# Kernel optimization log

Hardware: AMD Instinct MI355X
Metric: run time of the kernel (lower is better)

## Reference

```python
import jax, jax.numpy as jnp
import numpy as np

N = 50000          # total nodes
B = 10             # graphs in batch
NPG = N // B       # nodes per graph (equal-sized graphs)
E = 800000         # edges
IN_DIM = 128
HID = 128
NHEAD = 4
DHEAD = HID // NHEAD
T = 1000
SLOPE = 0.2        # leaky_relu negative slope
ALPHA_L = 2.0


def _ln(x, g=None, b=None, eps=1e-5):
    mu = jnp.mean(x, axis=-1, keepdims=True)
    var = jnp.var(x, axis=-1, keepdims=True)
    y = (x - mu) * jax.lax.rsqrt(var + eps)
    if g is not None:
        y = y * g + b
    return y


def _gatv2(h, src, dst, Ws, Wd, a, b):
    # DGL GATv2Conv, share_weights=False, residual=False, bias=True, activation=gelu
    fs = (h @ Ws).reshape(N, NHEAD, DHEAD)
    fd = (h @ Wd).reshape(N, NHEAD, DHEAD)
    # per-edge attention logits [E, NHEAD]
    e = jnp.sum(jax.nn.leaky_relu(fs[src] + fd[dst], SLOPE) * a, axis=-1)
    # edge softmax grouped by destination node
    m = jax.ops.segment_max(e, dst, num_segments=N)
    ee = jnp.exp(e - m[dst])
    den = jax.ops.segment_sum(ee, dst, num_segments=N)
    alpha = ee / den[dst]                                  # [E, NHEAD]
    rst = jax.ops.segment_sum(alpha[..., None] * fs[src], dst, num_segments=N)
    rst = jax.nn.gelu(rst + b.reshape(1, NHEAD, DHEAD), approximate=False)
    return rst.reshape(N, HID)


def _forward(x, noise, sab, somab, time_emb,
             Ws0, Wd0, a0, b0, g0, be0,
             Ws1, Wd1, a1, b1, g1, be1,
             Wo1, bo1, Wo2, bo2, src, dst, t):
    # sample_q: statistics-matched signed noise
    miu = jnp.mean(x, axis=0)
    std = jnp.std(x, axis=0, ddof=1)          # torch.std is unbiased
    nz = _ln(noise) * std + miu
    nz = jnp.sign(x) * jnp.abs(nz)
    s1 = jnp.repeat(sab[t], NPG)[:, None]
    s2 = jnp.repeat(somab[t], NPG)[:, None]
    x_t = s1 * x + s2 * nz
    temb = jnp.repeat(time_emb[t], NPG, axis=0)
    # Denoising_Unet
    h = jnp.concatenate([x_t, temb], axis=1)   # [N, IN_DIM+HID]
    h = _ln(_gatv2(h, src, dst, Ws0, Wd0, a0, b0), g0, be0)
    h_in = h
    h = _gatv2(h, src, dst, Ws1, Wd1, a1, b1)
    h = _ln(h + h_in, g1, be1)                 # residual (shapes match)
    out = jax.nn.relu(h @ Wo1 + bo1) @ Wo2 + bo2
    # loss_fn
    mse = jnp.mean((out - x) ** 2)
    on = out / jnp.maximum(jnp.linalg.norm(out, axis=-1, keepdims=True), 1e-12)
    xn = x / jnp.maximum(jnp.linalg.norm(x, axis=-1, keepdims=True), 1e-12)
    cos = jnp.mean((1.0 - jnp.sum(on * xn, axis=-1)) ** ALPHA_L)
    return mse + 0.1 * cos


def setup_inputs() -> dict:
    key = jax.random.key(0)
    ks = jax.random.split(key, 26)
    betas = np.linspace(1e-4, 0.02, T, dtype=np.float64)
    ab = np.cumprod(1.0 - betas)
    s = 0.02
    in0 = IN_DIM + HID
    inp = {}
    inp['x'] = jax.random.normal(ks[0], (N, IN_DIM), jnp.float32)
    inp['noise'] = jax.random.normal(ks[1], (N, IN_DIM), jnp.float32)
    inp['src'] = jax.random.randint(ks[2], (E,), 0, N, dtype=jnp.int32)
    inp['dst'] = jax.random.randint(ks[3], (E,), 0, N, dtype=jnp.int32)
    inp['t'] = jax.random.randint(ks[4], (B,), 0, T, dtype=jnp.int32)
    inp['sab'] = jnp.asarray(np.sqrt(ab), jnp.float32)
    inp['somab'] = jnp.asarray(np.sqrt(1.0 - ab), jnp.float32)
    inp['time_emb'] = jax.random.normal(ks[5], (T, HID), jnp.float32) * s
    inp['Ws0'] = jax.random.normal(ks[6], (in0, HID), jnp.float32) * s
    inp['Wd0'] = jax.random.normal(ks[7], (in0, HID), jnp.float32) * s
    inp['a0'] = jax.random.normal(ks[8], (NHEAD, DHEAD), jnp.float32) * s
    inp['b0'] = jnp.zeros((HID,), jnp.float32)
    inp['g0'] = jnp.ones((HID,), jnp.float32)
    inp['be0'] = jnp.zeros((HID,), jnp.float32)
    inp['Ws1'] = jax.random.normal(ks[9], (HID, HID), jnp.float32) * s
    inp['Wd1'] = jax.random.normal(ks[10], (HID, HID), jnp.float32) * s
    inp['a1'] = jax.random.normal(ks[11], (NHEAD, DHEAD), jnp.float32) * s
    inp['b1'] = jnp.zeros((HID,), jnp.float32)
    inp['g1'] = jnp.ones((HID,), jnp.float32)
    inp['be1'] = jnp.zeros((HID,), jnp.float32)
    inp['Wo1'] = jax.random.normal(ks[12], (HID, HID), jnp.float32) * s
    inp['bo1'] = jnp.zeros((HID,), jnp.float32)
    inp['Wo2'] = jax.random.normal(ks[13], (HID, IN_DIM), jnp.float32) * s
    inp['bo2'] = jnp.zeros((IN_DIM,), jnp.float32)
    return inp


def reference(x, noise, src, dst, t, sab, somab, time_emb,
              Ws0, Wd0, a0, b0, g0, be0,
              Ws1, Wd1, a1, b1, g1, be1,
              Wo1, bo1, Wo2, bo2):
    return _forward(x, noise, sab, somab, time_emb,
                    Ws0, Wd0, a0, b0, g0, be0,
                    Ws1, Wd1, a1, b1, g1, be1,
                    Wo1, bo1, Wo2, bo2, src, dst, t)
```

## Files before the change

kernel.cpp:

```cpp
#include <hip/hip_runtime.h>
#include <hip/hip_bf16.h>
#include <math.h>

#define NN 50000
#define EE 800000
#define NPG 5000

typedef short bf16x8 __attribute__((ext_vector_type(8)));
typedef float f32x4 __attribute__((ext_vector_type(4)));

__device__ __forceinline__ float gelu_exact(float v) {
    return 0.5f * v * (1.0f + erff(v * 0.70710678118654752440f));
}

__device__ __forceinline__ ushort f2b(float f) {
    union { float f; uint u; } v; v.f = f;
    uint r = (v.u + 0x7fffu + ((v.u >> 16) & 1)) >> 16;
    return (ushort)r;
}
__device__ __forceinline__ uint pack2(float a, float b) {
    return (uint)f2b(a) | ((uint)f2b(b) << 16);
}
__device__ __forceinline__ float blo(uint u) {
    union { uint u; float f; } v; v.u = u << 16; return v.f;
}
__device__ __forceinline__ float bhi(uint u) {
    union { uint u; float f; } v; v.u = u & 0xffff0000u; return v.f;
}
__device__ __forceinline__ void unpack8(uint4 u, float* f) {
    f[0] = blo(u.x); f[1] = bhi(u.x); f[2] = blo(u.y); f[3] = bhi(u.y);
    f[4] = blo(u.z); f[5] = bhi(u.z); f[6] = blo(u.w); f[7] = bhi(u.w);
}

__global__ __launch_bounds__(256) void head1_kernel(const float* __restrict__ x,
        float* __restrict__ sums, const int* __restrict__ dst, int* __restrict__ counts,
        const float* __restrict__ Ws0, const float* __restrict__ Wd0,
        const float* __restrict__ Ws1, const float* __restrict__ Wd1,
        const float* __restrict__ Wo1, const float* __restrict__ Wo2,
        ushort* __restrict__ Wt0, ushort* __restrict__ Wt1,
        ushort* __restrict__ Wo1t, ushort* __restrict__ Wo2t) {
    int bid = blockIdx.x;
    int tid = threadIdx.x;
    if (bid < 1024) {
        int col4 = (tid & 31) * 4;
        int rowgrp = tid >> 5;
        float s0 = 0.f, s1 = 0.f, s2 = 0.f, s3 = 0.f;
        float q0 = 0.f, q1 = 0.f, q2 = 0.f, q3 = 0.f;
        for (int r = bid * 8 + rowgrp; r < NN; r += 8192) {
            float4 v = *(const float4*)(x + (size_t)r * 128 + col4);
            s0 += v.x; s1 += v.y; s2 += v.z; s3 += v.w;
            q0 += v.x * v.x; q1 += v.y * v.y; q2 += v.z * v.z; q3 += v.w * v.w;
        }
        s0 += __shfl_xor(s0, 32); s1 += __shfl_xor(s1, 32);
        s2 += __shfl_xor(s2, 32); s3 += __shfl_xor(s3, 32);
        q0 += __shfl_xor(q0, 32); q1 += __shfl_xor(q1, 32);
        q2 += __shfl_xor(q2, 32); q3 += __shfl_xor(q3, 32);
        __shared__ float red[4][32][8];
        int wv = tid >> 6, l = tid & 63;
        if (l < 32) {
            float* p = red[wv][l];
            p[0] = s0; p[1] = s1; p[2] = s2; p[3] = s3;
            p[4] = q0; p[5] = q1; p[6] = q2; p[7] = q3;
        }
        __syncthreads();
        if (tid < 32) {
            float a0 = 0.f, a1 = 0.f, a2 = 0.f, a3 = 0.f;
            float b0 = 0.f, b1 = 0.f, b2 = 0.f, b3 = 0.f;
#pragma unroll
            for (int w = 0; w < 4; ++w) {
                float* p = red[w][tid];
                a0 += p[0]; a1 += p[1]; a2 += p[2]; a3 += p[3];
                b0 += p[4]; b1 += p[5]; b2 += p[6]; b3 += p[7];
            }
            int c = tid * 4;
            atomicAdd(&sums[c], a0); atomicAdd(&sums[c + 1], a1);
            atomicAdd(&sums[c + 2], a2); atomicAdd(&sums[c + 3], a3);
            atomicAdd(&sums[128 + c], b0); atomicAdd(&sums[128 + c + 1], b1);
            atomicAdd(&sums[128 + c + 2], b2); atomicAdd(&sums[128 + c + 3], b3);
        }
    } else if (bid < 4149) {
        int i = (bid - 1024) * 256 + tid;
        if (i < EE) atomicAdd(&counts[dst[i]], 1);
    } else {
        int i = (bid - 4149) * 256 + tid;
        if (i < 65536) {
            int c = i >> 8, k = i & 255;
            const float* W = (c < 128) ? Ws0 : Wd0;
            Wt0[c * 256 + k] = f2b(W[k * 128 + (c & 127)]);
        } else if (i < 98304) {
            int j = i - 65536;
            int c = j >> 7, k = j & 127;
            const float* W = (c < 128) ? Ws1 : Wd1;
            Wt1[c * 128 + k] = f2b(W[k * 128 + (c & 127)]);
        } else if (i < 114688) {
            int j = i - 98304;
            int c = j >> 7, k = j & 127;
            Wo1t[c * 128 + k] = f2b(Wo1[k * 128 + c]);
        } else if (i < 131072) {
            int j = i - 114688;
            int c = j >> 7, k = j & 127;
            Wo2t[c * 128 + k] = f2b(Wo2[k * 128 + c]);
        }
    }
}

__global__ __launch_bounds__(1024) void head2_kernel(const int* __restrict__ counts,
        int* __restrict__ blockSums, float* __restrict__ stats, int n) {
    int bid = blockIdx.x;
    int tid = threadIdx.x;
    if (bid < 49) {
        int i = bid * 1024 + tid;
        int v = (i < n) ? counts[i] : 0;
#pragma unroll
        for (int o = 32; o > 0; o >>= 1) v += __shfl_down(v, o);
        __shared__ int sh[16];
        int lane = tid & 63, wv = tid >> 6;
        if (lane == 0) sh[wv] = v;
        __syncthreads();
        if (tid == 0) {
            int s = 0;
#pragma unroll
            for (int k = 0; k < 16; ++k) s += sh[k];
            blockSums[bid] = s;
        }
    } else {
        if (tid < 128) {
            int c = tid;
            float sum = stats[c], sumsq = stats[128 + c];
            float mu = sum / (float)n;
            float var = (sumsq - sum * sum / (float)n) / (float)(n - 1);
            stats[256 + c] = mu;
            stats[384 + c] = sqrtf(fmaxf(var, 0.f));
        }
    }
}

__global__ __launch_bounds__(1024) void head3_kernel(const float* __restrict__ x,
        const float* __restrict__ noise, const int* __restrict__ t,
        const float* __restrict__ sab, const float* __restrict__ somab,
        const float* __restrict__ temb, const float* __restrict__ stats,
        ushort* __restrict__ h,
        const int* __restrict__ counts, const int* __restrict__ blockSums,
        int* __restrict__ indptr, int* __restrict__ cursor, int n) {
    int bid = blockIdx.x;
    int tid = threadIdx.x;
    if (bid < 3125) {
        int wid = bid * 16 + (tid >> 6);
        int lane = tid & 63;
        int tt = t[wid / NPG];
        float s1 = sab[tt], s2v = somab[tt];
        float2 nz = ((const float2*)noise)[(size_t)wid * 64 + lane];
        float s = nz.x + nz.y;
        float sq = nz.x * nz.x + nz.y * nz.y;
#pragma unroll
        for (int o = 1; o < 64; o <<= 1) { s += __shfl_xor(s, o); sq += __shfl_xor(sq, o); }
        float mu = s * (1.f / 128.f);
        float var = sq * (1.f / 128.f) - mu * mu;
        float r = rsqrtf(var + 1e-5f);
        int f0 = 2 * lane, f1 = f0 + 1;
        float y0 = (nz.x - mu) * r * stats[384 + f0] + stats[256 + f0];
        float y1 = (nz.y - mu) * r * stats[384 + f1] + stats[256 + f1];
        float2 xv = ((const float2*)x)[(size_t)wid * 64 + lane];
        float sg0 = (xv.x > 0.f) ? 1.f : ((xv.x < 0.f) ? -1.f : 0.f);
        float sg1 = (xv.y > 0.f) ? 1.f : ((xv.y < 0.f) ? -1.f : 0.f);
        float n0 = sg0 * fabsf(y0);
        float n1 = sg1 * fabsf(y1);
        float xt0 = s1 * xv.x + s2v * n0;
        float xt1 = s1 * xv.y + s2v * n1;
        uint* row = (uint*)(h + (size_t)wid * 256);
        row[lane] = pack2(xt0, xt1);
        float2 te = ((const float2*)(temb + (size_t)tt * 128))[lane];
        row[64 + lane] = pack2(te.x, te.y);
    } else {
        int b = bid - 3125;
        __shared__ int sOff, sTot;
        if (tid < 64) {
            int v = (tid < 49) ? blockSums[tid] : 0;
            int incl = v;
#pragma unroll
            for (int o = 1; o < 64; o <<= 1) {
                int tv = __shfl_up(incl, o);
                if ((tid & 63) >= o) incl += tv;
            }
            int off = (b == 0) ? 0 : __shfl(incl, b - 1);
            int tot = __shfl(incl, 48);
            if (tid == 0) { sOff = off; sTot = tot; }
        }
        __syncthreads();
        int i = b * 1024 + tid;
        int v = (i < n) ? counts[i] : 0;
        int lane = tid & 63, wv = tid >> 6;
        int incl = v;
#pragma unroll
        for (int o = 1; o < 64; o <<= 1) {
            int tv = __shfl_up(incl, o);
            if (lane >= o) incl += tv;
        }
        __shared__ int wsum[16];
        __shared__ int woff[16];
        if (lane == 63) wsum[wv] = incl;
        __syncthreads();
        if (tid == 0) {
            int s = 0;
#pragma unroll
            for (int k = 0; k < 16; ++k) { woff[k] = s; s += wsum[k]; }
        }
        __syncthreads();
        int ex = incl - v + woff[wv] + sOff;
        if (i < n) { indptr[i] = ex; cursor[i] = ex; }
        if (b == 48 && tid == 0) indptr[n] = sTot;
    }
}

__global__ __launch_bounds__(1024) void scatter_kernel(const int* __restrict__ src,
        const int* __restrict__ dst, int* __restrict__ cursor,
        int* __restrict__ csr_src, int e) {
    int i = blockIdx.x * 1024 + threadIdx.x;
    if (i < e) {
        int p = atomicAdd(&cursor[dst[i]], 1);
        csr_src[p] = src[i];
    }
}

template<int K, int NCOL, int EPI>
__global__ __launch_bounds__(256, 2) void mfma_gemm(const ushort* __restrict__ A,
        const ushort* __restrict__ Wt, const float* __restrict__ bias,
        ushort* __restrict__ C0, ushort* __restrict__ C1,
        const float* __restrict__ X, float* __restrict__ lossAcc, int M) {
    constexpr int NFRAG = NCOL / 16;
    constexpr int KSTEPS = K / 32;
    __shared__ ushort Bs[32 * NCOL];
    int tid = threadIdx.x;
    int wave = tid >> 6, lane = tid & 63;
    int l15 = lane & 15, g = lane >> 4;
    int rowBase = blockIdx.x * 64 + wave * 16;
    int r = rowBase + l15;
    int rc = min(r, M - 1);
    const ushort* Arow = A + (size_t)rc * K + g * 8;

    f32x4 acc[NFRAG] = {};

    for (int ks = 0; ks < KSTEPS; ++ks) {
#pragma unroll
        for (int i = 0; i < NCOL / 64; ++i) {
            int ch = tid + i * 256;
            int c = ch >> 2, q = ch & 3;
            float4 v = *(const float4*)(Wt + (size_t)c * K + ks * 32 + q * 8);
            int off = c * 64 + ((q * 16) ^ ((c & 7) << 4));
            *(float4*)((char*)Bs + off) = v;
        }
        __syncthreads();
        bf16x8 af = *(const bf16x8*)(Arow + ks * 32);
        int roff = l15 * 64 + ((g * 16) ^ ((l15 & 7) << 4));
#pragma unroll
        for (int n = 0; n < NFRAG; ++n) {
            bf16x8 bf = *(const bf16x8*)((const char*)Bs + n * 1024 + roff);
            acc[n] = __builtin_amdgcn_mfma_f32_16x16x32_bf16(af, bf, acc[n], 0, 0, 0);
        }
        __syncthreads();
    }

    if (EPI != 3) {
#pragma unroll
        for (int n = 0; n < NFRAG; ++n) {
            int col = n * 16 + l15;
#pragma unroll
            for (int j = 0; j < 4; ++j) {
                int row = rowBase + g * 4 + j;
                if (row < M) {
                    float v = acc[n][j];
                    if (EPI == 1) v = fmaxf(v + bias[col], 0.f);
                    ushort bv = f2b(v);
                    if (NCOL == 256) {
                        if (n < 8) C0[(size_t)row * 128 + col] = bv;
                        else       C1[(size_t)row * 128 + col - 128] = bv;
                    } else {
                        C0[(size_t)row * 128 + col] = bv;
                    }
                }
            }
        }
    } else {
        float td2 = 0.f, tcl = 0.f;
#pragma unroll
        for (int j = 0; j < 4; ++j) {
            int row = rowBase + g * 4 + j;
            bool rv = row < M;
            float d2 = 0.f, oo = 0.f, xx = 0.f, ox = 0.f;
#pragma unroll
            for (int n = 0; n < NFRAG; ++n) {
                int col = n * 16 + l15;
                float o = rv ? (acc[n][j] + bias[col]) : 0.f;
                float xv = rv ? X[(size_t)row * 128 + col] : 0.f;
                float e = o - xv;
                d2 += e * e; oo += o * o; xx += xv * xv; ox += o * xv;
            }
#pragma unroll
            for (int off = 1; off < 16; off <<= 1) {
                d2 += __shfl_xor(d2, off); oo += __shfl_xor(oo, off);
                xx += __shfl_xor(xx, off); ox += __shfl_xor(ox, off);
            }
            if (rv) {
                float no = fmaxf(sqrtf(oo), 1e-12f);
                float nx = fmaxf(sqrtf(xx), 1e-12f);
                float cs = 1.f - ox / (no * nx);
                td2 += d2; tcl += cs * cs;
            }
        }
        __shared__ float sd2[16], scl[16];
        if (l15 == 0) { sd2[wave * 4 + g] = td2; scl[wave * 4 + g] = tcl; }
        __syncthreads();
        if (tid == 0) {
            float a2 = 0.f, ac = 0.f;
#pragma unroll
            for (int k2 = 0; k2 < 16; ++k2) { a2 += sd2[k2]; ac += scl[k2]; }
            atomicAdd(&lossAcc[0], a2);
            atomicAdd(&lossAcc[1], ac);
        }
    }
}

__global__ __launch_bounds__(256) void gat_ln_kernel(const ushort* __restrict__ fs,
        const ushort* __restrict__ fd, const float* __restrict__ a,
        const float* __restrict__ bias, const int* __restrict__ indptr,
        const int* __restrict__ csr_src, const ushort* __restrict__ residB,
        const float* __restrict__ g, const float* __restrict__ be,
        ushort* __restrict__ outB, int n) {
    int wid = (blockIdx.x * blockDim.x + threadIdx.x) >> 6;
    int lane = threadIdx.x & 63;
    if (wid >= n) return;
    int quad = lane >> 4, s = lane & 15;
    int beg = indptr[wid], cnt = indptr[wid + 1] - beg;
    const int* ip = csr_src + beg;
    const uint4* fs4 = (const uint4*)fs;

    uint4 fdq = ((const uint4*)fd)[(size_t)wid * 16 + s];
    float fdv[8]; unpack8(fdq, fdv);
    float av[8];
    {
        float4 a0 = *(const float4*)(a + 8 * s);
        float4 a1 = *(const float4*)(a + 8 * s + 4);
        av[0] = a0.x; av[1] = a0.y; av[2] = a0.z; av[3] = a0.w;
        av[4] = a1.x; av[5] = a1.y; av[6] = a1.z; av[7] = a1.w;
    }

    int i0 = (quad < cnt) ? ip[quad] : 0;
    int i1 = (4 + quad < cnt) ? ip[4 + quad] : 0;
    uint4 vA = fs4[(size_t)i0 * 16 + s];
    uint4 vB = fs4[(size_t)i1 * 16 + s];
    int p0 = (8  < cnt) ? ip[8]  : 0;
    int p1 = (9  < cnt) ? ip[9]  : 0;
    int p2 = (10 < cnt) ? ip[10] : 0;
    int p3 = (11 < cnt) ? ip[11] : 0;

    float den = 0.f;
    float acc[8] = {};
    for (int j = 0; j < cnt; j += 4) {
        uint4 cur = vA; vA = vB;
        int pe = (quad == 0) ? p0 : (quad == 1) ? p1 : (quad == 2) ? p2 : p3;
        vB = fs4[(size_t)pe * 16 + s];
        p0 = (j + 12 < cnt) ? ip[j + 12] : 0;
        p1 = (j + 13 < cnt) ? ip[j + 13] : 0;
        p2 = (j + 14 < cnt) ? ip[j + 14] : 0;
        p3 = (j + 15 < cnt) ? ip[j + 15] : 0;
        float c[8]; unpack8(cur, c);
        float p = 0.f;
#pragma unroll
        for (int i = 0; i < 8; ++i) {
            float tv = c[i] + fdv[i];
            tv = (tv > 0.f) ? tv : 0.2f * tv;
            p = fmaf(tv, av[i], p);
        }
        p += __shfl_xor(p, 1);
        p += __shfl_xor(p, 2);
        float w = (j + quad < cnt) ? __expf(p) : 0.f;
        den += w;
#pragma unroll
        for (int i = 0; i < 8; ++i) acc[i] = fmaf(w, c[i], acc[i]);
    }
#pragma unroll
    for (int i = 0; i < 8; ++i) {
        acc[i] += __shfl_xor(acc[i], 16);
        acc[i] += __shfl_xor(acc[i], 32);
    }
    den += __shfl_xor(den, 16);
    den += __shfl_xor(den, 32);
    float inv = (cnt > 0) ? 1.f / den : 0.f;

    float bi[8];
    {
        float4 b0v = *(const float4*)(bias + 8 * s);
        float4 b1v = *(const float4*)(bias + 8 * s + 4);
        bi[0] = b0v.x; bi[1] = b0v.y; bi[2] = b0v.z; bi[3] = b0v.w;
        bi[4] = b1v.x; bi[5] = b1v.y; bi[6] = b1v.z; bi[7] = b1v.w;
    }
    float r[8];
#pragma unroll
    for (int i = 0; i < 8; ++i) r[i] = gelu_exact(acc[i] * inv + bi[i]);
    if (residB) {
        uint4 rq = ((const uint4*)residB)[(size_t)wid * 16 + s];
        float rv[8]; unpack8(rq, rv);
#pragma unroll
        for (int i = 0; i < 8; ++i) r[i] += rv[i];
    }
    float ssum = 0.f, ssq = 0.f;
#pragma unroll
    for (int i = 0; i < 8; ++i) { ssum += r[i]; ssq += r[i] * r[i]; }
#pragma unroll
    for (int o = 1; o < 16; o <<= 1) { ssum += __shfl_xor(ssum, o); ssq += __shfl_xor(ssq, o); }
    float mu = ssum * (1.f / 128.f);
    float var = ssq * (1.f / 128.f) - mu * mu;
    float rstd = rsqrtf(var + 1e-5f);
    float gv[8], bv[8];
    {
        float4 g0v = *(const float4*)(g + 8 * s);
        float4 g1v = *(const float4*)(g + 8 * s + 4);
        gv[0] = g0v.x; gv[1] = g0v.y; gv[2] = g0v.z; gv[3] = g0v.w;
        gv[4] = g1v.x; gv[5] = g1v.y; gv[6] = g1v.z; gv[7] = g1v.w;
        float4 e0v = *(const float4*)(be + 8 * s);
        float4 e1v = *(const float4*)(be + 8 * s + 4);
        bv[0] = e0v.x; bv[1] = e0v.y; bv[2] = e0v.z; bv[3] = e0v.w;
        bv[4] = e1v.x; bv[5] = e1v.y; bv[6] = e1v.z; bv[7] = e1v.w;
    }
    float o_[8];
#pragma unroll
    for (int i = 0; i < 8; ++i) o_[i] = (r[i] - mu) * rstd * gv[i] + bv[i];
    if (quad == 0) {
        uint4 w4;
        w4.x = pack2(o_[0], o_[1]); w4.y = pack2(o_[2], o_[3]);
        w4.z = pack2(o_[4], o_[5]); w4.w = pack2(o_[6], o_[7]);
        ((uint4*)outB)[(size_t)wid * 16 + s] = w4;
    }
}

__global__ void loss_final2(const float* __restrict__ lossAcc, float* __restrict__ outp, int n) {
    outp[0] = lossAcc[0] / ((float)n * 128.f) + 0.1f * (lossAcc[1] / (float)n);
}

extern "C" void kernel_launch(void* const* d_in, const int* in_sizes, int n_in,
                              void* d_out, int out_size, void* d_ws, size_t ws_size,
                              hipStream_t stream) {
    const int N = NN, E = EE;
    const float* x     = (const float*)d_in[0];
    const float* noise = (const float*)d_in[1];
    const int*   src   = (const int*)d_in[2];
    const int*   dst   = (const int*)d_in[3];
    const int*   t     = (const int*)d_in[4];
    const float* sab   = (const float*)d_in[5];
    const float* somab = (const float*)d_in[6];
    const float* temb  = (const float*)d_in[7];
    const float* Ws0   = (const float*)d_in[8];
    const float* Wd0   = (const float*)d_in[9];
    const float* a0    = (const float*)d_in[10];
    const float* b0    = (const float*)d_in[11];
    const float* g0    = (const float*)d_in[12];
    const float* be0   = (const float*)d_in[13];
    const float* Ws1   = (const float*)d_in[14];
    const float* Wd1   = (const float*)d_in[15];
    const float* a1    = (const float*)d_in[16];
    const float* b1    = (const float*)d_in[17];
    const float* g1    = (const float*)d_in[18];
    const float* be1   = (const float*)d_in[19];
    const float* Wo1   = (const float*)d_in[20];
    const float* bo1   = (const float*)d_in[21];
    const float* Wo2   = (const float*)d_in[22];
    const float* bo2   = (const float*)d_in[23];

    float* ws = (float*)d_ws;
    ushort* hB  = (ushort*)ws;
    ushort* Pb  = (ushort*)ws;
    ushort* fsB = (ushort*)(ws + (size_t)N * 128);
    ushort* fdB = (ushort*)(ws + (size_t)N * 192);
    ushort* Qb  = fdB;
    ushort* z   = fsB;
    float* wtail = ws + (size_t)N * 384;
    ushort* Wt0  = (ushort*)wtail;
    ushort* Wt1  = (ushort*)(wtail + 32768);
    ushort* Wo1t = (ushort*)(wtail + 49152);
    ushort* Wo2t = (ushort*)(wtail + 57344);
    float* stats    = wtail + 65536;
    float* lossAcc  = stats + 512;
    int* counts  = (int*)(lossAcc + 2048);
    int* indptr  = counts + N;
    int* cursor  = indptr + N + 1;
    int* csr_src = cursor + N;
    int* blockSums = csr_src + E;

    hipMemsetAsync(stats, 0, 514 * sizeof(float), stream);
    hipMemsetAsync(counts, 0, (size_t)N * sizeof(int), stream);

    head1_kernel<<<4661, 256, 0, stream>>>(x, stats, dst, counts,
                                           Ws0, Wd0, Ws1, Wd1, Wo1, Wo2,
                                           Wt0, Wt1, Wo1t, Wo2t);
    head2_kernel<<<50, 1024, 0, stream>>>(counts, blockSums, stats, N);
    head3_kernel<<<3174, 1024, 0, stream>>>(x, noise, t, sab, somab, temb, stats, hB,
                                            counts, blockSums, indptr, cursor, N);
    scatter_kernel<<<(E + 1023) / 1024, 1024, 0, stream>>>(src, dst, cursor, csr_src, E);

    int gemmGrid = (N + 63) / 64;
    mfma_gemm<256, 256, 0><<<gemmGrid, 256, 0, stream>>>(hB, Wt0, nullptr, fsB, fdB,
                                                         nullptr, nullptr, N);
    gat_ln_kernel<<<(N + 3) / 4, 256, 0, stream>>>(fsB, fdB, a0, b0, indptr, csr_src,
                                                   nullptr, g0, be0, Pb, N);
    mfma_gemm<128, 256, 0><<<gemmGrid, 256, 0, stream>>>(Pb, Wt1, nullptr, fsB, fdB,
                                                         nullptr, nullptr, N);
    gat_ln_kernel<<<(N + 3) / 4, 256, 0, stream>>>(fsB, fdB, a1, b1, indptr, csr_src,
                                                   Pb, g1, be1, Qb, N);
    mfma_gemm<128, 128, 1><<<gemmGrid, 256, 0, stream>>>(Qb, Wo1t, bo1, z, nullptr,
                                                         nullptr, nullptr, N);
    mfma_gemm<128, 128, 3><<<gemmGrid, 256, 0, stream>>>(z, Wo2t, bo2, nullptr, nullptr,
                                                         x, lossAcc, N);
    loss_final2<<<1, 1, 0, stream>>>(lossAcc, (float*)d_out, N);
}
```

Before: 400.7 us.

## Store gathered source features as FP8 and fuse output MLP with loss

The GEMM now writes the source projection (fs) as FP8 e4m3 instead of bf16, which halves the bytes the per-edge gather in the GAT kernel has to read. The GAT kernel is reorganised so each lane handles 16 channels and 8 edges are processed per step. The two output GEMMs and the loss reduction are merged into one kernel that keeps the intermediate activation in shared memory, saving one launch and a global round trip. The cost is lower precision on the gathered features, which may move the loss away from the reference.

```diff
diff --git a/kernel.cpp b/kernel.cpp
--- a/kernel.cpp
+++ b/kernel.cpp
@@ -8,6 +8,13 @@
 
 typedef short bf16x8 __attribute__((ext_vector_type(8)));
 typedef float f32x4 __attribute__((ext_vector_type(4)));
+typedef float f32x2 __attribute__((ext_vector_type(2)));
+
+#if __has_builtin(__builtin_amdgcn_cvt_pk_f32_fp8) && __has_builtin(__builtin_amdgcn_cvt_pk_fp8_f32)
+#define HWFP8 1
+#else
+#define HWFP8 0
+#endif
 
 __device__ __forceinline__ float gelu_exact(float v) {
     return 0.5f * v * (1.0f + erff(v * 0.70710678118654752440f));
@@ -30,6 +37,63 @@
 __device__ __forceinline__ void unpack8(uint4 u, float* f) {
     f[0] = blo(u.x); f[1] = bhi(u.x); f[2] = blo(u.y); f[3] = bhi(u.y);
     f[4] = blo(u.z); f[5] = bhi(u.z); f[6] = blo(u.w); f[7] = bhi(u.w);
+}
+__device__ __forceinline__ void load16f(const float* p, float* out) {
+#pragma unroll
+    for (int i = 0; i < 4; ++i) {
+        float4 t = *(const float4*)(p + 4 * i);
+        out[4 * i] = t.x; out[4 * i + 1] = t.y; out[4 * i + 2] = t.z; out[4 * i + 3] = t.w;
+    }
+}
+
+__device__ __forceinline__ uchar f2fp8_sw(float f) {
+    uint u = __float_as_uint(f);
+    uint sign = (u >> 24) & 0x80u;
+    uint absu = u & 0x7fffffffu;
+    if (absu >= 0x43e00000u) return (uchar)(sign | 0x7eu);
+    int e32 = (int)(absu >> 23);
+    if (e32 < 121) {
+        float af = __uint_as_float(absu);
+        uint m = (uint)__float2int_rn(af * 512.f);
+        return (uchar)(sign | m);
+    }
+    uint mant = absu & 0x7fffffu;
+    uint keep = mant >> 20;
+    uint rest = mant & 0xfffffu;
+    uint rnd = (rest > 0x80000u || (rest == 0x80000u && (keep & 1u))) ? 1u : 0u;
+    uint code = (((uint)(e32 - 120) << 3) | keep) + rnd;
+    if (code > 0x7eu) code = 0x7eu;
+    return (uchar)(sign | code);
+}
+__device__ __forceinline__ float fp82f_sw(uint b) {
+    uint em = b & 0x7fu;
+    uint s = (b & 0x80u) << 24;
+    float norm = __uint_as_float(s | (((em >> 3) + 120u) << 23) | ((em & 7u) << 20));
+    float sub = __uint_as_float(s | 0x3F800000u) * (float)(int)em * 0.001953125f;
+    return (em >= 8u) ? norm : sub;
+}
+__device__ __forceinline__ uchar enc1(float v) {
+#if HWFP8
+    return (uchar)(__builtin_amdgcn_cvt_pk_fp8_f32(v, v, 0, false) & 0xff);
+#else
+    return f2fp8_sw(v);
+#endif
+}
+__device__ __forceinline__ void dec16(uint4 u, float* f) {
+#pragma unroll
+    for (int i = 0; i < 4; ++i) {
+        uint w = (&u.x)[i];
+#if HWFP8
+        f32x2 lo = __builtin_amdgcn_cvt_pk_f32_fp8((int)w, false);
+        f32x2 hi = __builtin_amdgcn_cvt_pk_f32_fp8((int)w, true);
+        f[4 * i] = lo.x; f[4 * i + 1] = lo.y; f[4 * i + 2] = hi.x; f[4 * i + 3] = hi.y;
+#else
+        f[4 * i]     = fp82f_sw(w & 0xffu);
+        f[4 * i + 1] = fp82f_sw((w >> 8) & 0xffu);
+        f[4 * i + 2] = fp82f_sw((w >> 16) & 0xffu);
+        f[4 * i + 3] = fp82f_sw((w >> 24) & 0xffu);
+#endif
+    }
 }
 
 __global__ __launch_bounds__(256) void head1_kernel(const float* __restrict__ x,
@@ -222,27 +286,26 @@
     }
 }
 
-template<int K, int NCOL, int EPI>
+template<int K>
 __global__ __launch_bounds__(256, 2) void mfma_gemm(const ushort* __restrict__ A,
-        const ushort* __restrict__ Wt, const float* __restrict__ bias,
-        ushort* __restrict__ C0, ushort* __restrict__ C1,
-        const float* __restrict__ X, float* __restrict__ lossAcc, int M) {
-    constexpr int NFRAG = NCOL / 16;
+        const ushort* __restrict__ Wt, uchar* __restrict__ C8,
+        ushort* __restrict__ C1, int M) {
+    constexpr int NCOL = 256;
+    constexpr int NFRAG = 16;
     constexpr int KSTEPS = K / 32;
     __shared__ ushort Bs[32 * NCOL];
     int tid = threadIdx.x;
     int wave = tid >> 6, lane = tid & 63;
     int l15 = lane & 15, g = lane >> 4;
     int rowBase = blockIdx.x * 64 + wave * 16;
-    int r = rowBase + l15;
-    int rc = min(r, M - 1);
+    int rc = min(rowBase + l15, M - 1);
     const ushort* Arow = A + (size_t)rc * K + g * 8;
 
     f32x4 acc[NFRAG] = {};
 
     for (int ks = 0; ks < KSTEPS; ++ks) {
 #pragma unroll
-        for (int i = 0; i < NCOL / 64; ++i) {
+        for (int i = 0; i < 4; ++i) {
             int ch = tid + i * 256;
             int c = ch >> 2, q = ch & 3;
             float4 v = *(const float4*)(Wt + (size_t)c * K + ks * 32 + q * 8);
@@ -260,67 +323,22 @@
         __syncthreads();
     }
 
-    if (EPI != 3) {
-#pragma unroll
-        for (int n = 0; n < NFRAG; ++n) {
-            int col = n * 16 + l15;
-#pragma unroll
-            for (int j = 0; j < 4; ++j) {
-                int row = rowBase + g * 4 + j;
-                if (row < M) {
-                    float v = acc[n][j];
-                    if (EPI == 1) v = fmaxf(v + bias[col], 0.f);
-                    ushort bv = f2b(v);
-                    if (NCOL == 256) {
-                        if (n < 8) C0[(size_t)row * 128 + col] = bv;
-                        else       C1[(size_t)row * 128 + col - 128] = bv;
-                    } else {
-                        C0[(size_t)row * 128 + col] = bv;
-                    }
-                }
-            }
-        }
-    } else {
-        float td2 = 0.f, tcl = 0.f;
+#pragma unroll
+    for (int n = 0; n < NFRAG; ++n) {
+        int col = n * 16 + l15;
 #pragma unroll
         for (int j = 0; j < 4; ++j) {
             int row = rowBase + g * 4 + j;
-            bool rv = row < M;
-            float d2 = 0.f, oo = 0.f, xx = 0.f, ox = 0.f;
-#pragma unroll
-            for (int n = 0; n < NFRAG; ++n) {
-                int col = n * 16 + l15;
-                float o = rv ? (acc[n][j] + bias[col]) : 0.f;
-                float xv = rv ? X[(size_t)row * 128 + col] : 0.f;
-                float e = o - xv;
-                d2 += e * e; oo += o * o; xx += xv * xv; ox += o * xv;
+            if (row < M) {
+                float v = acc[n][j];
+                if (n < 8) C8[(size_t)row * 128 + col] = enc1(v);
+                else       C1[(size_t)row * 128 + col - 128] = f2b(v);
             }
-#pragma unroll
-            for (int off = 1; off < 16; off <<= 1) {
-                d2 += __shfl_xor(d2, off); oo += __shfl_xor(oo, off);
-                xx += __shfl_xor(xx, off); ox += __shfl_xor(ox, off);
-            }
-            if (rv) {
-                float no = fmaxf(sqrtf(oo), 1e-12f);
-                float nx = fmaxf(sqrtf(xx), 1e-12f);
-                float cs = 1.f - ox / (no * nx);
-                td2 += d2; tcl += cs * cs;
-            }
-        }
-        __shared__ float sd2[16], scl[16];
-        if (l15 == 0) { sd2[wave * 4 + g] = td2; scl[wave * 4 + g] = tcl; }
-        __syncthreads();
-        if (tid == 0) {
-            float a2 = 0.f, ac = 0.f;
-#pragma unroll
-            for (int k2 = 0; k2 < 16; ++k2) { a2 += sd2[k2]; ac += scl[k2]; }
-            atomicAdd(&lossAcc[0], a2);
-            atomicAdd(&lossAcc[1], ac);
-        }
-    }
-}
-
-__global__ __launch_bounds__(256) void gat_ln_kernel(const ushort* __restrict__ fs,
+        }
+    }
+}
+
+__global__ __launch_bounds__(256) void gat_ln_kernel(const uchar* __restrict__ fs8,
         const ushort* __restrict__ fd, const float* __restrict__ a,
         const float* __restrict__ bias, const int* __restrict__ indptr,
         const int* __restrict__ csr_src, const ushort* __restrict__ residB,
@@ -329,107 +347,191 @@
     int wid = (blockIdx.x * blockDim.x + threadIdx.x) >> 6;
     int lane = threadIdx.x & 63;
     if (wid >= n) return;
-    int quad = lane >> 4, s = lane & 15;
+    int o = lane >> 3, s = lane & 7;
     int beg = indptr[wid], cnt = indptr[wid + 1] - beg;
     const int* ip = csr_src + beg;
-    const uint4* fs4 = (const uint4*)fs;
-
-    uint4 fdq = ((const uint4*)fd)[(size_t)wid * 16 + s];
-    float fdv[8]; unpack8(fdq, fdv);
-    float av[8];
+    const uint4* fs4 = (const uint4*)fs8;
+
+    float fdv[16], av[16];
     {
-        float4 a0 = *(const float4*)(a + 8 * s);
-        float4 a1 = *(const float4*)(a + 8 * s + 4);
-        av[0] = a0.x; av[1] = a0.y; av[2] = a0.z; av[3] = a0.w;
-        av[4] = a1.x; av[5] = a1.y; av[6] = a1.z; av[7] = a1.w;
-    }
-
-    int i0 = (quad < cnt) ? ip[quad] : 0;
-    int i1 = (4 + quad < cnt) ? ip[4 + quad] : 0;
-    uint4 vA = fs4[(size_t)i0 * 16 + s];
-    uint4 vB = fs4[(size_t)i1 * 16 + s];
-    int p0 = (8  < cnt) ? ip[8]  : 0;
-    int p1 = (9  < cnt) ? ip[9]  : 0;
-    int p2 = (10 < cnt) ? ip[10] : 0;
-    int p3 = (11 < cnt) ? ip[11] : 0;
+        uint4 q0 = ((const uint4*)fd)[(size_t)wid * 16 + 2 * s];
+        uint4 q1 = ((const uint4*)fd)[(size_t)wid * 16 + 2 * s + 1];
+        unpack8(q0, fdv); unpack8(q1, fdv + 8);
+        load16f(a + 16 * s, av);
+    }
+
+    int ia = (o < cnt) ? ip[o] : 0;
+    int ib = (8 + o < cnt) ? ip[8 + o] : 0;
+    uint4 vA = fs4[(size_t)ia * 8 + s];
+    uint4 vB = fs4[(size_t)ib * 8 + s];
 
     float den = 0.f;
-    float acc[8] = {};
-    for (int j = 0; j < cnt; j += 4) {
+    float acc[16] = {};
+    for (int j = 0; j < cnt; j += 8) {
         uint4 cur = vA; vA = vB;
-        int pe = (quad == 0) ? p0 : (quad == 1) ? p1 : (quad == 2) ? p2 : p3;
-        vB = fs4[(size_t)pe * 16 + s];
-        p0 = (j + 12 < cnt) ? ip[j + 12] : 0;
-        p1 = (j + 13 < cnt) ? ip[j + 13] : 0;
-        p2 = (j + 14 < cnt) ? ip[j + 14] : 0;
-        p3 = (j + 15 < cnt) ? ip[j + 15] : 0;
-        float c[8]; unpack8(cur, c);
+        int ic = (j + 16 + o < cnt) ? ip[j + 16 + o] : 0;
+        vB = fs4[(size_t)ic * 8 + s];
+        float c[16];
+        dec16(cur, c);
         float p = 0.f;
 #pragma unroll
-        for (int i = 0; i < 8; ++i) {
+        for (int i = 0; i < 16; ++i) {
             float tv = c[i] + fdv[i];
             tv = (tv > 0.f) ? tv : 0.2f * tv;
             p = fmaf(tv, av[i], p);
         }
         p += __shfl_xor(p, 1);
-        p += __shfl_xor(p, 2);
-        float w = (j + quad < cnt) ? __expf(p) : 0.f;
+        float w = (j + o < cnt) ? __expf(p) : 0.f;
         den += w;
 #pragma unroll
-        for (int i = 0; i < 8; ++i) acc[i] = fmaf(w, c[i], acc[i]);
-    }
-#pragma unroll
-    for (int i = 0; i < 8; ++i) {
+        for (int i = 0; i < 16; ++i) acc[i] = fmaf(w, c[i], acc[i]);
+    }
+#pragma unroll
+    for (int i = 0; i < 16; ++i) {
+        acc[i] += __shfl_xor(acc[i], 8);
         acc[i] += __shfl_xor(acc[i], 16);
         acc[i] += __shfl_xor(acc[i], 32);
     }
+    den += __shfl_xor(den, 8);
     den += __shfl_xor(den, 16);
     den += __shfl_xor(den, 32);
     float inv = (cnt > 0) ? 1.f / den : 0.f;
 
-    float bi[8];
-    {
-        float4 b0v = *(const float4*)(bias + 8 * s);
-        float4 b1v = *(const float4*)(bias + 8 * s + 4);
-        bi[0] = b0v.x; bi[1] = b0v.y; bi[2] = b0v.z; bi[3] = b0v.w;
-        bi[4] = b1v.x; bi[5] = b1v.y; bi[6] = b1v.z; bi[7] = b1v.w;
-    }
-    float r[8];
-#pragma unroll
-    for (int i = 0; i < 8; ++i) r[i] = gelu_exact(acc[i] * inv + bi[i]);
+    float bi[16];
+    load16f(bias + 16 * s, bi);
+    float r[16];
+#pragma unroll
+    for (int i = 0; i < 16; ++i) r[i] = gelu_exact(acc[i] * inv + bi[i]);
     if (residB) {
-        uint4 rq = ((const uint4*)residB)[(size_t)wid * 16 + s];
-        float rv[8]; unpack8(rq, rv);
-#pragma unroll
-        for (int i = 0; i < 8; ++i) r[i] += rv[i];
+        uint4 q0 = ((const uint4*)residB)[(size_t)wid * 16 + 2 * s];
+        uint4 q1 = ((const uint4*)residB)[(size_t)wid * 16 + 2 * s + 1];
+        float rv[16]; unpack8(q0, rv); unpack8(q1, rv + 8);
+#pragma unroll
+        for (int i = 0; i < 16; ++i) r[i] += rv[i];
     }
     float ssum = 0.f, ssq = 0.f;
 #pragma unroll
-    for (int i = 0; i < 8; ++i) { ssum += r[i]; ssq += r[i] * r[i]; }
-#pragma unroll
-    for (int o = 1; o < 16; o <<= 1) { ssum += __shfl_xor(ssum, o); ssq += __shfl_xor(ssq, o); }
+    for (int i = 0; i < 16; ++i) { ssum += r[i]; ssq += r[i] * r[i]; }
+#pragma unroll
+    for (int off = 1; off < 8; off <<= 1) {
+        ssum += __shfl_xor(ssum, off); ssq += __shfl_xor(ssq, off);
+    }
     float mu = ssum * (1.f / 128.f);
     float var = ssq * (1.f / 128.f) - mu * mu;
     float rstd = rsqrtf(var + 1e-5f);
-    float gv[8], bv[8];
-    {
-        float4 g0v = *(const float4*)(g + 8 * s);
-        float4 g1v = *(const float4*)(g + 8 * s + 4);
-        gv[0] = g0v.x; gv[1] = g0v.y; gv[2] = g0v.z; gv[3] = g0v.w;
-        gv[4] = g1v.x; gv[5] = g1v.y; gv[6] = g1v.z; gv[7] = g1v.w;
-        float4 e0v = *(const float4*)(be + 8 * s);
-        float4 e1v = *(const float4*)(be + 8 * s + 4);
-        bv[0] = e0v.x; bv[1] = e0v.y; bv[2] = e0v.z; bv[3] = e0v.w;
-        bv[4] = e1v.x; bv[5] = e1v.y; bv[6] = e1v.z; bv[7] = e1v.w;
-    }
-    float o_[8];
-#pragma unroll
-    for (int i = 0; i < 8; ++i) o_[i] = (r[i] - mu) * rstd * gv[i] + bv[i];
-    if (quad == 0) {
-        uint4 w4;
-        w4.x = pack2(o_[0], o_[1]); w4.y = pack2(o_[2], o_[3]);
-        w4.z = pack2(o_[4], o_[5]); w4.w = pack2(o_[6], o_[7]);
-        ((uint4*)outB)[(size_t)wid * 16 + s] = w4;
+    float gv[16], bv[16];
+    load16f(g + 16 * s, gv);
+    load16f(be + 16 * s, bv);
+    float o_[16];
+#pragma unroll
+    for (int i = 0; i < 16; ++i) o_[i] = (r[i] - mu) * rstd * gv[i] + bv[i];
+    if (o == 0) {
+        uint4 w0, w1;
+        w0.x = pack2(o_[0], o_[1]);  w0.y = pack2(o_[2], o_[3]);
+        w0.z = pack2(o_[4], o_[5]);  w0.w = pack2(o_[6], o_[7]);
+        w1.x = pack2(o_[8], o_[9]);  w1.y = pack2(o_[10], o_[11]);
+        w1.z = pack2(o_[12], o_[13]); w1.w = pack2(o_[14], o_[15]);
+        ((uint4*)outB)[(size_t)wid * 16 + 2 * s] = w0;
+        ((uint4*)outB)[(size_t)wid * 16 + 2 * s + 1] = w1;
+    }
+}
+
+__global__ __launch_bounds__(256, 2) void mlp_loss_kernel(const ushort* __restrict__ Qb,
+        const ushort* __restrict__ Wo1t, const ushort* __restrict__ Wo2t,
+        const float* __restrict__ bo1, const float* __restrict__ bo2,
+        const float* __restrict__ X, float* __restrict__ lossAcc, int M) {
+    __shared__ ushort W1[16384];
+    __shared__ ushort W2[16384];
+    __shared__ ushort Zt[8192];
+    int tid = threadIdx.x;
+    int wave = tid >> 6, lane = tid & 63;
+    int l15 = lane & 15, g = lane >> 4;
+#pragma unroll
+    for (int it = 0; it < 8; ++it) {
+        int q = (it * 256 + tid) * 16;
+        int col = q >> 8, qk = q & 255;
+        int srcb = (col << 8) + (qk ^ ((col & 7) << 4));
+        *(float4*)((char*)W1 + q) = *(const float4*)((const char*)Wo1t + srcb);
+        *(float4*)((char*)W2 + q) = *(const float4*)((const char*)Wo2t + srcb);
+    }
+    int rowBase = blockIdx.x * 64 + wave * 16;
+    int rc = min(rowBase + l15, M - 1);
+    const ushort* Arow = Qb + (size_t)rc * 128 + g * 8;
+    f32x4 acc1[8] = {};
+    __syncthreads();
+#pragma unroll
+    for (int ks = 0; ks < 4; ++ks) {
+        bf16x8 af = *(const bf16x8*)(Arow + ks * 32);
+#pragma unroll
+        for (int n = 0; n < 8; ++n) {
+            int col = n * 16 + l15;
+            int boff = (col << 8) + ((ks * 64 + g * 16) ^ ((col & 7) << 4));
+            bf16x8 bf = *(const bf16x8*)((const char*)W1 + boff);
+            acc1[n] = __builtin_amdgcn_mfma_f32_16x16x32_bf16(af, bf, acc1[n], 0, 0, 0);
+        }
+    }
+#pragma unroll
+    for (int n = 0; n < 8; ++n) {
+        int col = n * 16 + l15;
+        float bv = bo1[col];
+#pragma unroll
+        for (int j = 0; j < 4; ++j) {
+            int lr = wave * 16 + g * 4 + j;
+            float v = fmaxf(acc1[n][j] + bv, 0.f);
+            int zoff = (lr << 8) + ((col * 2) ^ ((lr & 7) << 4));
+            *(ushort*)((char*)Zt + zoff) = f2b(v);
+        }
+    }
+    __syncthreads();
+    f32x4 acc2[8] = {};
+    int lr = wave * 16 + l15;
+#pragma unroll
+    for (int ks = 0; ks < 4; ++ks) {
+        int aoff = (lr << 8) + ((ks * 64 + g * 16) ^ ((lr & 7) << 4));
+        bf16x8 af = *(const bf16x8*)((const char*)Zt + aoff);
+#pragma unroll
+        for (int n = 0; n < 8; ++n) {
+            int col = n * 16 + l15;
+            int boff = (col << 8) + ((ks * 64 + g * 16) ^ ((col & 7) << 4));
+            bf16x8 bf = *(const bf16x8*)((const char*)W2 + boff);
+            acc2[n] = __builtin_amdgcn_mfma_f32_16x16x32_bf16(af, bf, acc2[n], 0, 0, 0);
+        }
+    }
+    float td2 = 0.f, tcl = 0.f;
+#pragma unroll
+    for (int j = 0; j < 4; ++j) {
+        int row = rowBase + g * 4 + j;
+        bool rv = row < M;
+        float d2 = 0.f, oo = 0.f, xx = 0.f, ox = 0.f;
+#pragma unroll
+        for (int n = 0; n < 8; ++n) {
+            int col = n * 16 + l15;
+            float ov = rv ? (acc2[n][j] + bo2[col]) : 0.f;
+            float xv = rv ? X[(size_t)row * 128 + col] : 0.f;
+            float e = ov - xv;
+            d2 += e * e; oo += ov * ov; xx += xv * xv; ox += ov * xv;
+        }
+#pragma unroll
+        for (int off = 1; off < 16; off <<= 1) {
+            d2 += __shfl_xor(d2, off); oo += __shfl_xor(oo, off);
+            xx += __shfl_xor(xx, off); ox += __shfl_xor(ox, off);
+        }
+        if (rv) {
+            float no = fmaxf(sqrtf(oo), 1e-12f);
+            float nx = fmaxf(sqrtf(xx), 1e-12f);
+            float cs = 1.f - ox / (no * nx);
+            td2 += d2; tcl += cs * cs;
+        }
+    }
+    __shared__ float sd2[16], scl[16];
+    if (l15 == 0) { sd2[wave * 4 + g] = td2; scl[wave * 4 + g] = tcl; }
+    __syncthreads();
+    if (tid == 0) {
+        float a2 = 0.f, ac = 0.f;
+#pragma unroll
+        for (int k2 = 0; k2 < 16; ++k2) { a2 += sd2[k2]; ac += scl[k2]; }
+        atomicAdd(&lossAcc[0], a2);
+        atomicAdd(&lossAcc[1], ac);
     }
 }
 
@@ -469,10 +571,9 @@
     float* ws = (float*)d_ws;
     ushort* hB  = (ushort*)ws;
     ushort* Pb  = (ushort*)ws;
-    ushort* fsB = (ushort*)(ws + (size_t)N * 128);
+    uchar*  fs8 = (uchar*)(ws + (size_t)N * 128);
     ushort* fdB = (ushort*)(ws + (size_t)N * 192);
     ushort* Qb  = fdB;
-    ushort* z   = fsB;
     float* wtail = ws + (size_t)N * 384;
     ushort* Wt0  = (ushort*)wtail;
     ushort* Wt1  = (ushort*)(wtail + 32768);
@@ -498,17 +599,12 @@
     scatter_kernel<<<(E + 1023) / 1024, 1024, 0, stream>>>(src, dst, cursor, csr_src, E);
 
     int gemmGrid = (N + 63) / 64;
-    mfma_gemm<256, 256, 0><<<gemmGrid, 256, 0, stream>>>(hB, Wt0, nullptr, fsB, fdB,
-                                                         nullptr, nullptr, N);
-    gat_ln_kernel<<<(N + 3) / 4, 256, 0, stream>>>(fsB, fdB, a0, b0, indptr, csr_src,
+    mfma_gemm<256><<<gemmGrid, 256, 0, stream>>>(hB, Wt0, fs8, fdB, N);
+    gat_ln_kernel<<<(N + 3) / 4, 256, 0, stream>>>(fs8, fdB, a0, b0, indptr, csr_src,
                                                    nullptr, g0, be0, Pb, N);
-    mfma_gemm<128, 256, 0><<<gemmGrid, 256, 0, stream>>>(Pb, Wt1, nullptr, fsB, fdB,
-                                                         nullptr, nullptr, N);
-    gat_ln_kernel<<<(N + 3) / 4, 256, 0, stream>>>(fsB, fdB, a1, b1, indptr, csr_src,
+    mfma_gemm<128><<<gemmGrid, 256, 0, stream>>>(Pb, Wt1, fs8, fdB, N);
+    gat_ln_kernel<<<(N + 3) / 4, 256, 0, stream>>>(fs8, fdB, a1, b1, indptr, csr_src,
                                                    Pb, g1, be1, Qb, N);
-    mfma_gemm<128, 128, 1><<<gemmGrid, 256, 0, stream>>>(Qb, Wo1t, bo1, z, nullptr,
-                                                         nullptr, nullptr, N);
-    mfma_gemm<128, 128, 3><<<gemmGrid, 256, 0, stream>>>(z, Wo2t, bo2, nullptr, nullptr,
-                                                         x, lossAcc, N);
+    mlp_loss_kernel<<<gemmGrid, 256, 0, stream>>>(Qb, Wo1t, Wo2t, bo1, bo2, x, lossAcc, N);
     loss_final2<<<1, 1, 0, stream>>>(lossAcc, (float*)d_out, N);
 }
```

Result: slower. 461.5 us (+15.2%).
